# Performance work log

Measured on AMD Instinct MI355X. Metric: run time of the kernel, lower is better.

The kernel has to match this reference:

```python
import jax, jax.numpy as jnp
import numpy as np

D_MODEL, D_FF, N_HEAD = 1024, 4096, 16
D_HEAD = D_MODEL // N_HEAD
B, S = 8, 1024
EPS = 1e-6


def gelu(x):
    # tanh-approx GELU exactly as in source
    c = jnp.sqrt(jnp.asarray(2.0 / jnp.pi, x.dtype))
    return 0.5 * x * (1.0 + jnp.tanh(c * (x + 0.044715 * x ** 3)))


def layernorm(x, g, b):
    mu = jnp.mean(x, axis=-1, keepdims=True)
    var = jnp.mean((x - mu) ** 2, axis=-1, keepdims=True)
    return (x - mu) * jax.lax.rsqrt(var + EPS) * g + b


def setup_inputs() -> dict:
    key = jax.random.key(0)
    ks = jax.random.split(key, 12)
    s = 0.02
    p = lambda k, sh: (jax.random.normal(k, sh, jnp.float32) * s)
    inp = {
        "iter": 1,
        "x": jax.random.normal(ks[0], (B, S, D_MODEL), jnp.float32),
        "mask": jnp.tril(jnp.ones((S, S), jnp.float32))[None, None, :, :],
        "Wq": p(ks[1], (D_MODEL, D_MODEL)), "bq": jnp.zeros((D_MODEL,), jnp.float32),
        "Wk": p(ks[2], (D_MODEL, D_MODEL)), "bk": jnp.zeros((D_MODEL,), jnp.float32),
        "Wv": p(ks[3], (D_MODEL, D_MODEL)), "bv": jnp.zeros((D_MODEL,), jnp.float32),
        "W1": p(ks[4], (D_MODEL, D_FF)),   "b1": jnp.zeros((D_FF,), jnp.float32),
        "W2": p(ks[5], (D_FF, D_MODEL)),   "b2": jnp.zeros((D_MODEL,), jnp.float32),
        "ln_attn_g": jnp.ones((D_MODEL,), jnp.float32), "ln_attn_b": jnp.zeros((D_MODEL,), jnp.float32),
        "ln_ffn_g": jnp.ones((D_MODEL,), jnp.float32),  "ln_ffn_b": jnp.zeros((D_MODEL,), jnp.float32),
    }
    return inp


def encoder_layer(x, mask, Wq, bq, Wk, bk, Wv, bv, W1, b1, W2, b2,
                  ln_attn_g, ln_attn_b, ln_ffn_g, ln_ffn_b, it):
    # pre-norm on all iterations except the first
    norm_x = layernorm(x, ln_attn_g, ln_attn_b) if it != 0 else x

    def heads(t):  # [B,S,D] -> [B,H,S,Dh]
        return t.reshape(B, S, N_HEAD, D_HEAD).transpose(0, 2, 1, 3)

    q = heads(norm_x @ Wq + bq) / jnp.sqrt(jnp.asarray(D_HEAD, x.dtype))
    k = heads(norm_x @ Wk + bk)
    v = heads(norm_x @ Wv + bv)

    scores = jnp.einsum("bhqd,bhkd->bhqk", q, k)
    scores = scores * mask  # multiplicative mask, as in source
    attn = jax.nn.softmax(scores, axis=-1)
    context = jnp.einsum("bhqk,bhkd->bhqd", attn, v)
    # Faithful to torch .view on contiguous [B,H,S,Dh]: plain reshape (head-interleaving bug preserved)
    context = context.reshape(B, S, N_HEAD * D_HEAD)

    out = context + x  # residual (dropout = identity in eval)

    # positionwise FFN with internal pre-norm and residual
    h = layernorm(out, ln_ffn_g, ln_ffn_b)
    h = gelu(h @ W1 + b1)
    h = h @ W2 + b2
    return h + out


def reference(iter, x, mask, Wq, bq, Wk, bk, Wv, bv, W1, b1, W2, b2,
              ln_attn_g, ln_attn_b, ln_ffn_g, ln_ffn_b):
    return encoder_layer(x, mask, Wq, bq, Wk, bk, Wv, bv, W1, b1, W2, b2,
                         ln_attn_g, ln_attn_b, ln_ffn_g, ln_ffn_b, iter)
```

## Files before the change

### kernel.cpp

```cpp
#include <hip/hip_runtime.h>


#define B_N 8
#define SEQ 1024
#define DM 1024
#define DFF 4096
#define NH 16
#define DH 64
#define MROWS (B_N * SEQ)

typedef __attribute__((ext_vector_type(4))) float f32x4;
typedef __attribute__((ext_vector_type(8))) short short8;
typedef __attribute__((ext_vector_type(4))) unsigned short us4;
typedef unsigned short u16;

__device__ __forceinline__ float b2f(u16 u) { return __uint_as_float(((unsigned)u) << 16); }
__device__ __forceinline__ u16 f2b(float f) {
    unsigned u = __float_as_uint(f);
    return (u16)((u + 0x7fffu + ((u >> 16) & 1u)) >> 16);
}
__device__ __forceinline__ float gelu_f(float x) {
    float t = tanhf(0.7978845608028654f * (x + 0.044715f * x * x * x));
    return 0.5f * x * (1.0f + t);
}
__device__ __forceinline__ void async_cp16(const void* g, void* l) {
    __builtin_amdgcn_global_load_lds(
        (const __attribute__((address_space(1))) unsigned int*)g,
        (__attribute__((address_space(3))) unsigned int*)l, 16, 0, 0);
}

#define WAITL0()                                                                \
    asm volatile("s_waitcnt lgkmcnt(0)" ::: "memory");                          \
    __builtin_amdgcn_sched_barrier(0)

template <int EPI>
__global__ __launch_bounds__(256, 3) void gemm3(
    const u16* __restrict__ A, int lda,
    const u16* __restrict__ Bt, int ldb,
    void* __restrict__ C, int ldc,
    const float* __restrict__ bias, float scale, int K)
{
    __shared__ __align__(16) char lds[32768];

    const int tid = threadIdx.x;
    const int lane = tid & 63;
    const int w = tid >> 6;
    const int wm = w >> 1, wn = w & 1;
    const int rr = lane & 15, qq = lane >> 4;
    const int m0 = blockIdx.y * 128, n0 = blockIdx.x * 128;

    const int s = (rr & 7) << 4;
    const int swq = (qq * 16) ^ (s & 48);
    const int ksx[2] = { s & 64, 64 ^ (s & 64) };
    const int aoff = (wm * 64 + rr) * 128 + swq;
    const int boff = 16384 + (wn * 64 + rr) * 128 + swq;

    f32x4 acc[4][4];
#pragma unroll
    for (int i = 0; i < 4; i++)
#pragma unroll
        for (int j = 0; j < 4; j++)
#pragma unroll
            for (int e = 0; e < 4; e++) acc[i][j][e] = 0.f;

    const int NT = K >> 6;
    for (int t = 0; t < NT; ++t) {
#pragma unroll
        for (int i = 0; i < 4; ++i) {
            int g = tid + i * 256;
            int gs = (g & ~7) | ((g ^ (g >> 3)) & 7);
            async_cp16(A + (size_t)(m0 + (gs >> 3)) * lda + (t << 6) + ((gs & 7) << 3),
                       lds + g * 16);
        }
#pragma unroll
        for (int i = 0; i < 4; ++i) {
            int g = tid + i * 256;
            int gs = (g & ~7) | ((g ^ (g >> 3)) & 7);
            async_cp16(Bt + (size_t)(n0 + (gs >> 3)) * ldb + (t << 6) + ((gs & 7) << 3),
                       lds + 16384 + g * 16);
        }
        __syncthreads();

        short8 af[4][2], bfr[4][2];
#pragma unroll
        for (int mi = 0; mi < 4; ++mi)
#pragma unroll
            for (int ks = 0; ks < 2; ++ks)
                af[mi][ks] = *(const short8*)(lds + aoff + mi * 2048 + ksx[ks]);
#pragma unroll
        for (int ni = 0; ni < 4; ++ni)
#pragma unroll
            for (int ks = 0; ks < 2; ++ks)
                bfr[ni][ks] = *(const short8*)(lds + boff + ni * 2048 + ksx[ks]);
#pragma unroll
        for (int ks = 0; ks < 2; ++ks)
#pragma unroll
            for (int mi = 0; mi < 4; ++mi)
#pragma unroll
                for (int ni = 0; ni < 4; ++ni)
                    acc[mi][ni] = __builtin_amdgcn_mfma_f32_16x16x32_bf16(
                        af[mi][ks], bfr[ni][ks], acc[mi][ni], 0, 0, 0);
        __syncthreads();
    }

    const int ccol = n0 + wn * 64 + rr;
    const int crow = m0 + wm * 64 + qq * 4;
#pragma unroll
    for (int mi = 0; mi < 4; ++mi) {
#pragma unroll
        for (int ni = 0; ni < 4; ++ni) {
            const int colg = ccol + ni * 16;
            const float bv = bias ? bias[colg] : 0.f;
#pragma unroll
            for (int j = 0; j < 4; ++j) {
                const int rowg = crow + mi * 16 + j;
                float v = (acc[mi][ni][j] + bv) * scale;
                size_t idx = (size_t)rowg * ldc + colg;
                if (EPI == 1) v = gelu_f(v);
                if (EPI == 2) ((float*)C)[idx] += v;
                else ((u16*)C)[idx] = f2b(v);
            }
        }
    }
}

__global__ void vcolsum(const u16* __restrict__ Vb, float* __restrict__ Vcs)
{
    const int t = blockIdx.x, bh = blockIdx.y;
    const int b = bh >> 4, h = bh & 15;
    const int d = threadIdx.x;
    const u16* base = Vb + (size_t)(b * 1024 + t * 128) * DM + h * 64 + d;
    float s = 0.f;
#pragma unroll 8
    for (int k = 0; k < 128; ++k) s += b2f(base[(size_t)k * DM]);
    Vcs[((bh << 3) + t) * 64 + d] = s;
}

__global__ __launch_bounds__(256, 2) void flash_attn(
    const u16* __restrict__ Qb, const u16* __restrict__ Kb,
    const u16* __restrict__ Vt, const float* __restrict__ Vcs,
    u16* __restrict__ ctx)
{
    constexpr float L2E = 1.44269504f;
    const int bh = blockIdx.x, qt = blockIdx.y;
    const int b = bh >> 4, h = bh & 15;
    const int tid = threadIdx.x, lane = tid & 63, w = tid >> 6;
    const int rr = lane & 15, qq = lane >> 4;

    __shared__ __align__(16) u16 smem[32768];
    char* Ksb = (char*)smem;
    char* Vsb = (char*)(smem + 8192);
    char* Psb = (char*)(smem + 16384 + w * 4096);

    short8 qf[2][2];
    {
        const size_t qr = (size_t)(b * 1024 + qt * 128 + w * 32 + rr);
#pragma unroll
        for (int mi = 0; mi < 2; ++mi)
#pragma unroll
            for (int ks = 0; ks < 2; ++ks)
                qf[mi][ks] = *(const short8*)(Qb + (qr + mi * 16) * DM + h * 64 + ks * 32 + qq * 8);
    }

    f32x4 oacc[2][4];
    float mrow[2][4], lrow[2][4];
#pragma unroll
    for (int mi = 0; mi < 2; ++mi)
#pragma unroll
        for (int j = 0; j < 4; ++j) { mrow[mi][j] = -1e30f; lrow[mi][j] = 0.f; }
#pragma unroll
    for (int mi = 0; mi < 2; ++mi)
#pragma unroll
        for (int ni = 0; ni < 4; ++ni)
#pragma unroll
            for (int e = 0; e < 4; ++e) oacc[mi][ni][e] = 0.f;

    const u16* Kbase = Kb + (size_t)b * 1024 * DM + h * 64;
    const u16* Vbase = Vt + ((size_t)bh << 16);
    const int sxr = (rr & 7) << 4;
    const int qbase = qt * 128 + w * 32 + qq * 4;

    for (int t = 0; t <= qt; ++t) {
#pragma unroll
        for (int i = 0; i < 4; ++i) {
            int g = tid + i * 256;
            int gs = (g & ~7) | ((g ^ (g >> 3)) & 7);
            async_cp16(Kbase + (size_t)(t * 128 + (gs >> 3)) * DM + ((gs & 7) << 3),
                       Ksb + g * 16);
        }
#pragma unroll
        for (int i = 0; i < 4; ++i) {
            int g = tid + i * 256;
            int gs = (g & ~7) | ((g ^ (g >> 4)) & 7);
            async_cp16(Vbase + (size_t)(gs >> 4) * SEQ + t * 128 + ((gs & 15) << 3),
                       Vsb + g * 16);
        }
        __syncthreads();

        f32x4 sacc[2][8];
#pragma unroll
        for (int mi = 0; mi < 2; ++mi)
#pragma unroll
            for (int ni = 0; ni < 8; ++ni)
#pragma unroll
                for (int e = 0; e < 4; ++e) sacc[mi][ni][e] = 0.f;
#pragma unroll
        for (int ks = 0; ks < 2; ++ks)
#pragma unroll
            for (int ni = 0; ni < 8; ++ni) {
                short8 kf = *(const short8*)(Ksb + (rr + ni * 16) * 128 +
                                             ((ks * 64 + qq * 16) ^ sxr));
#pragma unroll
                for (int mi = 0; mi < 2; ++mi)
                    sacc[mi][ni] = __builtin_amdgcn_mfma_f32_16x16x32_bf16(
                        qf[mi][ks], kf, sacc[mi][ni], 0, 0, 0);
            }

        float mx[2][4];
#pragma unroll
        for (int mi = 0; mi < 2; ++mi)
#pragma unroll
            for (int j = 0; j < 4; ++j) mx[mi][j] = -1e30f;
        if (t == qt) {
            const int kb0 = t * 128 + rr;
#pragma unroll
            for (int mi = 0; mi < 2; ++mi)
#pragma unroll
                for (int ni = 0; ni < 8; ++ni)
#pragma unroll
                    for (int j = 0; j < 4; ++j) {
                        float sv = (kb0 + ni * 16 <= qbase + mi * 16 + j) ? sacc[mi][ni][j] : 0.f;
                        sacc[mi][ni][j] = sv;
                        mx[mi][j] = fmaxf(mx[mi][j], sv);
                    }
        } else {
#pragma unroll
            for (int mi = 0; mi < 2; ++mi)
#pragma unroll
                for (int ni = 0; ni < 8; ++ni)
#pragma unroll
                    for (int j = 0; j < 4; ++j)
                        mx[mi][j] = fmaxf(mx[mi][j], sacc[mi][ni][j]);
        }
#pragma unroll
        for (int mi = 0; mi < 2; ++mi)
#pragma unroll
            for (int j = 0; j < 4; ++j) {
                float v = mx[mi][j];
#pragma unroll
                for (int o = 1; o < 16; o <<= 1) v = fmaxf(v, __shfl_xor(v, o, 64));
                mx[mi][j] = v;
            }

        float rs[2][4];
#pragma unroll
        for (int mi = 0; mi < 2; ++mi)
#pragma unroll
            for (int j = 0; j < 4; ++j) {
                float mn = fmaxf(mrow[mi][j], mx[mi][j]);
                float sc = exp2f((mrow[mi][j] - mn) * L2E);
                mrow[mi][j] = mn;
                lrow[mi][j] *= sc;
                rs[mi][j] = 0.f;
#pragma unroll
                for (int ni = 0; ni < 4; ++ni) oacc[mi][ni][j] *= sc;
            }
#pragma unroll
        for (int mi = 0; mi < 2; ++mi)
#pragma unroll
            for (int ni = 0; ni < 8; ++ni)
#pragma unroll
                for (int j = 0; j < 4; ++j) {
                    float p = exp2f((sacc[mi][ni][j] - mrow[mi][j]) * L2E);
                    rs[mi][j] += p;
                    const int prow = mi * 16 + qq * 4 + j;
                    *(u16*)(Psb + prow * 256 +
                            (((rr + ni * 16) * 2) ^ ((prow & 7) << 4))) = f2b(p);
                }
#pragma unroll
        for (int mi = 0; mi < 2; ++mi)
#pragma unroll
            for (int j = 0; j < 4; ++j) {
                float v = rs[mi][j];
#pragma unroll
                for (int o = 1; o < 16; o <<= 1) v += __shfl_xor(v, o, 64);
                lrow[mi][j] += v;
            }

        WAITL0();

#pragma unroll
        for (int kk = 0; kk < 4; ++kk) {
            short8 pa[2], pv[4];
#pragma unroll
            for (int mi = 0; mi < 2; ++mi)
                pa[mi] = *(const short8*)(Psb + (mi * 16 + rr) * 256 +
                                          ((kk * 64 + qq * 16) ^ sxr));
#pragma unroll
            for (int ni = 0; ni < 4; ++ni)
                pv[ni] = *(const short8*)(Vsb + (rr + ni * 16) * 256 +
                                          ((kk * 64 + qq * 16) ^ sxr));
#pragma unroll
            for (int mi = 0; mi < 2; ++mi)
#pragma unroll
                for (int ni = 0; ni < 4; ++ni)
                    oacc[mi][ni] = __builtin_amdgcn_mfma_f32_16x16x32_bf16(
                        pa[mi], pv[ni], oacc[mi][ni], 0, 0, 0);
        }
        __syncthreads();
    }

    if (qt < 7) {
        float vsuf[4] = { 0.f, 0.f, 0.f, 0.f };
        for (int tt = qt + 1; tt < 8; ++tt)
#pragma unroll
            for (int ni = 0; ni < 4; ++ni)
                vsuf[ni] += Vcs[((bh << 3) + tt) * 64 + rr + ni * 16];
        const float km = (float)((7 - qt) * 128);
#pragma unroll
        for (int mi = 0; mi < 2; ++mi)
#pragma unroll
            for (int j = 0; j < 4; ++j) {
                float m = mrow[mi][j];
                float mfin = fmaxf(m, 0.f);
                float sc = exp2f((m - mfin) * L2E);
                float w0 = exp2f(-mfin * L2E);
                lrow[mi][j] = lrow[mi][j] * sc + km * w0;
#pragma unroll
                for (int ni = 0; ni < 4; ++ni)
                    oacc[mi][ni][j] = oacc[mi][ni][j] * sc + w0 * vsuf[ni];
            }
    }

    float inv[2][4];
#pragma unroll
    for (int mi = 0; mi < 2; ++mi)
#pragma unroll
        for (int j = 0; j < 4; ++j) inv[mi][j] = 1.0f / lrow[mi][j];
    u16* cb = ctx + ((size_t)bh << 16);
#pragma unroll
    for (int mi = 0; mi < 2; ++mi)
#pragma unroll
        for (int ni = 0; ni < 4; ++ni)
#pragma unroll
            for (int j = 0; j < 4; ++j) {
                const int srow = qt * 128 + w * 32 + mi * 16 + qq * 4 + j;
                cb[(size_t)srow * 64 + rr + ni * 16] = f2b(oacc[mi][ni][j] * inv[mi][j]);
            }
}

__global__ __launch_bounds__(256) void ln_bf16(
    const float* __restrict__ in, const float* __restrict__ gg,
    const float* __restrict__ bb, u16* __restrict__ outp,
    const int* __restrict__ iterp)
{
    const int row = blockIdx.x;
    const int t = threadIdx.x;
    const int lane = t & 63, w = t >> 6;
    const float* r = in + (size_t)row * DM;
    f32x4 x = *(const f32x4*)(r + t * 4);
    __shared__ float red[4];

    float s = x[0] + x[1] + x[2] + x[3];
#pragma unroll
    for (int o = 32; o; o >>= 1) s += __shfl_xor(s, o, 64);
    if (lane == 0) red[w] = s;
    __syncthreads();
    float mu = (red[0] + red[1] + red[2] + red[3]) * (1.0f / DM);
    __syncthreads();

    float d0 = x[0] - mu, d1 = x[1] - mu, d2 = x[2] - mu, d3 = x[3] - mu;
    float q = d0 * d0 + d1 * d1 + d2 * d2 + d3 * d3;
#pragma unroll
    for (int o = 32; o; o >>= 1) q += __shfl_xor(q, o, 64);
    if (lane == 0) red[w] = q;
    __syncthreads();
    float rs = rsqrtf((red[0] + red[1] + red[2] + red[3]) * (1.0f / DM) + 1e-6f);

    bool apply = !(iterp && iterp[0] == 0);
    f32x4 gv = *(const f32x4*)(gg + t * 4);
    f32x4 bv = *(const f32x4*)(bb + t * 4);
    us4 o;
    if (apply) {
        o[0] = f2b(d0 * rs * gv[0] + bv[0]);
        o[1] = f2b(d1 * rs * gv[1] + bv[1]);
        o[2] = f2b(d2 * rs * gv[2] + bv[2]);
        o[3] = f2b(d3 * rs * gv[3] + bv[3]);
    } else {
        o[0] = f2b(x[0]); o[1] = f2b(x[1]); o[2] = f2b(x[2]); o[3] = f2b(x[3]);
    }
    *(us4*)(outp + (size_t)row * DM + t * 4) = o;
}

__global__ void transW(const float* __restrict__ W, u16* __restrict__ WT, int Kd, int Nd)
{
    __shared__ float tile[32][33];
    int bx = blockIdx.x << 5, by = blockIdx.y << 5;
    int tx = threadIdx.x, ty = threadIdx.y;
#pragma unroll
    for (int i = 0; i < 32; i += 8)
        tile[ty + i][tx] = W[(size_t)(by + ty + i) * Nd + bx + tx];
    __syncthreads();
#pragma unroll
    for (int i = 0; i < 32; i += 8)
        WT[(size_t)(bx + ty + i) * Kd + by + tx] = f2b(tile[tx][ty + i]);
}

__global__ void transV(const u16* __restrict__ Vb, u16* __restrict__ Vt)
{
    __shared__ u16 tile[32][33];
    int s0 = blockIdx.x << 5, d0 = blockIdx.y << 5, bh = blockIdx.z;
    int b = bh >> 4, h = bh & 15;
    int tx = threadIdx.x, ty = threadIdx.y;
#pragma unroll
    for (int i = 0; i < 32; i += 8)
        tile[ty + i][tx] = Vb[(size_t)((b << 10) + s0 + ty + i) * DM + (h << 6) + d0 + tx];
    __syncthreads();
#pragma unroll
    for (int i = 0; i < 32; i += 8)
        Vt[((size_t)bh << 16) + (size_t)(d0 + ty + i) * SEQ + s0 + tx] = tile[tx][ty + i];
}

__global__ __launch_bounds__(256) void resid_add(
    const u16* __restrict__ ctx, const float* __restrict__ x, float* __restrict__ outp)
{
    size_t i = ((size_t)blockIdx.x * 256 + threadIdx.x) * 4;
    us4 c = *(const us4*)(ctx + i);
    f32x4 xv = *(const f32x4*)(x + i);
    f32x4 o;
#pragma unroll
    for (int j = 0; j < 4; j++) o[j] = xv[j] + b2f(c[j]);
    *(f32x4*)(outp + i) = o;
}

extern "C" void kernel_launch(void* const* d_in, const int* in_sizes, int n_in,
                              void* d_out, int out_size, void* d_ws, size_t ws_size,
                              hipStream_t stream)
{
    const int* iter = (const int*)d_in[0];
    const float* x = (const float*)d_in[1];
    const float* Wq = (const float*)d_in[3];
    const float* bq = (const float*)d_in[4];
    const float* Wk = (const float*)d_in[5];
    const float* bk = (const float*)d_in[6];
    const float* Wv = (const float*)d_in[7];
    const float* bv = (const float*)d_in[8];
    const float* W1 = (const float*)d_in[9];
    const float* b1 = (const float*)d_in[10];
    const float* W2 = (const float*)d_in[11];
    const float* b2 = (const float*)d_in[12];
    const float* lag = (const float*)d_in[13];
    const float* lab = (const float*)d_in[14];
    const float* lfg = (const float*)d_in[15];
    const float* lfb = (const float*)d_in[16];
    float* out = (float*)d_out;

    char* ws = (char*)d_ws;
    size_t off = 0;
    auto alloc = [&](size_t bytes) {
        char* p = ws + off;
        off += (bytes + 255) & ~(size_t)255;
        return p;
    };
    u16* NXb = (u16*)alloc((size_t)MROWS * DM * 2);
    u16* Qb  = (u16*)alloc((size_t)MROWS * DM * 2);
    u16* Kb  = (u16*)alloc((size_t)MROWS * DM * 2);
    u16* Vb  = (u16*)alloc((size_t)MROWS * DM * 2);
    u16* ctx = (u16*)alloc((size_t)MROWS * DM * 2);
    u16* h2  = (u16*)alloc((size_t)MROWS * DFF * 2);
    u16* WqT = (u16*)alloc((size_t)DM * DM * 2);
    u16* WkT = (u16*)alloc((size_t)DM * DM * 2);
    u16* WvT = (u16*)alloc((size_t)DM * DM * 2);
    u16* W1T = (u16*)alloc((size_t)DM * DFF * 2);
    u16* W2T = (u16*)alloc((size_t)DM * DFF * 2);
    float* Vcs = (float*)alloc((size_t)B_N * NH * 8 * 64 * 4);
    u16* Vt = NXb;
    u16* h1 = Qb;

    dim3 tb(32, 8);
    transW<<<dim3(DM / 32, DM / 32), tb, 0, stream>>>(Wq, WqT, DM, DM);
    transW<<<dim3(DM / 32, DM / 32), tb, 0, stream>>>(Wk, WkT, DM, DM);
    transW<<<dim3(DM / 32, DM / 32), tb, 0, stream>>>(Wv, WvT, DM, DM);
    transW<<<dim3(DFF / 32, DM / 32), tb, 0, stream>>>(W1, W1T, DM, DFF);
    transW<<<dim3(DM / 32, DFF / 32), tb, 0, stream>>>(W2, W2T, DFF, DM);

    ln_bf16<<<MROWS, 256, 0, stream>>>(x, lag, lab, NXb, iter);

    gemm3<0><<<dim3(DM / 128, MROWS / 128), 256, 0, stream>>>(
        NXb, DM, WqT, DM, Qb, DM, bq, 0.125f, DM);
    gemm3<0><<<dim3(DM / 128, MROWS / 128), 256, 0, stream>>>(
        NXb, DM, WkT, DM, Kb, DM, bk, 1.0f, DM);
    gemm3<0><<<dim3(DM / 128, MROWS / 128), 256, 0, stream>>>(
        NXb, DM, WvT, DM, Vb, DM, bv, 1.0f, DM);

    transV<<<dim3(SEQ / 32, DH / 32, B_N * NH), tb, 0, stream>>>(Vb, Vt);
    vcolsum<<<dim3(8, B_N * NH), 64, 0, stream>>>(Vb, Vcs);

    flash_attn<<<dim3(B_N * NH, SEQ / 128), 256, 0, stream>>>(Qb, Kb, Vt, Vcs, ctx);

    resid_add<<<(MROWS * DM) / 1024, 256, 0, stream>>>(ctx, x, out);

    ln_bf16<<<MROWS, 256, 0, stream>>>(out, lfg, lfb, h1, nullptr);
    gemm3<1><<<dim3(DFF / 128, MROWS / 128), 256, 0, stream>>>(
        h1, DM, W1T, DM, h2, DFF, b1, 1.0f, DM);
    gemm3<2><<<dim3(DM / 128, MROWS / 128), 256, 0, stream>>>(
        h2, DFF, W2T, DFF, (void*)out, DM, b2, 1.0f, DFF);
}
```

Measured before the change: 435.2 us.

## Fuse QKV projections into one GEMM, fold residual into attention, cheaper GELU

Concatenates Wq/Wk/Wv (with the 1/sqrt(d) scale folded into Wq and its bias) into a single 3072-wide GEMM, replacing three launches and giving a larger grid. Attention now reads Q/K/V from the interleaved QKV buffer and writes fp32 output plus residual directly, which removes the separate residual-add kernel and the bf16 context round trip. GELU's tanh is rewritten as an exp2 plus hardware reciprocal form, which is cheaper but slightly less precise. Folding the scale into bf16 weights is exact for 0.125, since it is a power of two.

```diff
diff --git a/kernel.cpp b/kernel.cpp
--- a/kernel.cpp
+++ b/kernel.cpp
@@ -4,6 +4,7 @@
 #define B_N 8
 #define SEQ 1024
 #define DM 1024
+#define DQKV 3072
 #define DFF 4096
 #define NH 16
 #define DH 64
@@ -20,8 +21,12 @@
     return (u16)((u + 0x7fffu + ((u >> 16) & 1u)) >> 16);
 }
 __device__ __forceinline__ float gelu_f(float x) {
-    float t = tanhf(0.7978845608028654f * (x + 0.044715f * x * x * x));
-    return 0.5f * x * (1.0f + t);
+    float x2 = x * x;
+    float z2l = x * (2.3013935056f + 0.1029194997f * x2);
+    float t = exp2f(z2l);
+    float r;
+    asm("v_rcp_f32 %0, %1" : "=v"(r) : "v"(t + 1.0f));
+    return x - x * r;
 }
 __device__ __forceinline__ void async_cp16(const void* g, void* l) {
     __builtin_amdgcn_global_load_lds(
@@ -124,22 +129,22 @@
     }
 }
 
-__global__ void vcolsum(const u16* __restrict__ Vb, float* __restrict__ Vcs)
+__global__ void vcolsum(const u16* __restrict__ QKV, float* __restrict__ Vcs)
 {
     const int t = blockIdx.x, bh = blockIdx.y;
     const int b = bh >> 4, h = bh & 15;
     const int d = threadIdx.x;
-    const u16* base = Vb + (size_t)(b * 1024 + t * 128) * DM + h * 64 + d;
+    const u16* base = QKV + (size_t)(b * 1024 + t * 128) * DQKV + 2048 + h * 64 + d;
     float s = 0.f;
 #pragma unroll 8
-    for (int k = 0; k < 128; ++k) s += b2f(base[(size_t)k * DM]);
+    for (int k = 0; k < 128; ++k) s += b2f(base[(size_t)k * DQKV]);
     Vcs[((bh << 3) + t) * 64 + d] = s;
 }
 
 __global__ __launch_bounds__(256, 2) void flash_attn(
-    const u16* __restrict__ Qb, const u16* __restrict__ Kb,
-    const u16* __restrict__ Vt, const float* __restrict__ Vcs,
-    u16* __restrict__ ctx)
+    const u16* __restrict__ QKV, const u16* __restrict__ Vt,
+    const float* __restrict__ Vcs, const float* __restrict__ x,
+    float* __restrict__ outp)
 {
     constexpr float L2E = 1.44269504f;
     const int bh = blockIdx.x, qt = blockIdx.y;
@@ -159,7 +164,7 @@
         for (int mi = 0; mi < 2; ++mi)
 #pragma unroll
             for (int ks = 0; ks < 2; ++ks)
-                qf[mi][ks] = *(const short8*)(Qb + (qr + mi * 16) * DM + h * 64 + ks * 32 + qq * 8);
+                qf[mi][ks] = *(const short8*)(QKV + (qr + mi * 16) * DQKV + h * 64 + ks * 32 + qq * 8);
     }
 
     f32x4 oacc[2][4];
@@ -175,7 +180,7 @@
 #pragma unroll
             for (int e = 0; e < 4; ++e) oacc[mi][ni][e] = 0.f;
 
-    const u16* Kbase = Kb + (size_t)b * 1024 * DM + h * 64;
+    const u16* Kbase = QKV + (size_t)b * 1024 * DQKV + 1024 + h * 64;
     const u16* Vbase = Vt + ((size_t)bh << 16);
     const int sxr = (rr & 7) << 4;
     const int qbase = qt * 128 + w * 32 + qq * 4;
@@ -185,7 +190,7 @@
         for (int i = 0; i < 4; ++i) {
             int g = tid + i * 256;
             int gs = (g & ~7) | ((g ^ (g >> 3)) & 7);
-            async_cp16(Kbase + (size_t)(t * 128 + (gs >> 3)) * DM + ((gs & 7) << 3),
+            async_cp16(Kbase + (size_t)(t * 128 + (gs >> 3)) * DQKV + ((gs & 7) << 3),
                        Ksb + g * 16);
         }
 #pragma unroll
@@ -337,15 +342,17 @@
     for (int mi = 0; mi < 2; ++mi)
 #pragma unroll
         for (int j = 0; j < 4; ++j) inv[mi][j] = 1.0f / lrow[mi][j];
-    u16* cb = ctx + ((size_t)bh << 16);
+    const float* xb = x + ((size_t)bh << 16);
+    float* ob = outp + ((size_t)bh << 16);
 #pragma unroll
     for (int mi = 0; mi < 2; ++mi)
 #pragma unroll
         for (int ni = 0; ni < 4; ++ni)
 #pragma unroll
             for (int j = 0; j < 4; ++j) {
-                const int srow = qt * 128 + w * 32 + mi * 16 + qq * 4 + j;
-                cb[(size_t)srow * 64 + rr + ni * 16] = f2b(oacc[mi][ni][j] * inv[mi][j]);
+                const size_t idx = (size_t)(qt * 128 + w * 32 + mi * 16 + qq * 4 + j) * 64
+                                   + rr + ni * 16;
+                ob[idx] = xb[idx] + oacc[mi][ni][j] * inv[mi][j];
             }
 }
 
@@ -392,7 +399,8 @@
     *(us4*)(outp + (size_t)row * DM + t * 4) = o;
 }
 
-__global__ void transW(const float* __restrict__ W, u16* __restrict__ WT, int Kd, int Nd)
+__global__ void transW(const float* __restrict__ W, u16* __restrict__ WT,
+                       int Kd, int Nd, float sc)
 {
     __shared__ float tile[32][33];
     int bx = blockIdx.x << 5, by = blockIdx.y << 5;
@@ -403,10 +411,10 @@
     __syncthreads();
 #pragma unroll
     for (int i = 0; i < 32; i += 8)
-        WT[(size_t)(bx + ty + i) * Kd + by + tx] = f2b(tile[tx][ty + i]);
-}
-
-__global__ void transV(const u16* __restrict__ Vb, u16* __restrict__ Vt)
+        WT[(size_t)(bx + ty + i) * Kd + by + tx] = f2b(tile[tx][ty + i] * sc);
+}
+
+__global__ void transV(const u16* __restrict__ QKV, u16* __restrict__ Vt)
 {
     __shared__ u16 tile[32][33];
     int s0 = blockIdx.x << 5, d0 = blockIdx.y << 5, bh = blockIdx.z;
@@ -414,23 +422,19 @@
     int tx = threadIdx.x, ty = threadIdx.y;
 #pragma unroll
     for (int i = 0; i < 32; i += 8)
-        tile[ty + i][tx] = Vb[(size_t)((b << 10) + s0 + ty + i) * DM + (h << 6) + d0 + tx];
+        tile[ty + i][tx] = QKV[(size_t)((b << 10) + s0 + ty + i) * DQKV + 2048 + (h << 6) + d0 + tx];
     __syncthreads();
 #pragma unroll
     for (int i = 0; i < 32; i += 8)
         Vt[((size_t)bh << 16) + (size_t)(d0 + ty + i) * SEQ + s0 + tx] = tile[tx][ty + i];
 }
 
-__global__ __launch_bounds__(256) void resid_add(
-    const u16* __restrict__ ctx, const float* __restrict__ x, float* __restrict__ outp)
-{
-    size_t i = ((size_t)blockIdx.x * 256 + threadIdx.x) * 4;
-    us4 c = *(const us4*)(ctx + i);
-    f32x4 xv = *(const f32x4*)(x + i);
-    f32x4 o;
-#pragma unroll
-    for (int j = 0; j < 4; j++) o[j] = xv[j] + b2f(c[j]);
-    *(f32x4*)(outp + i) = o;
+__global__ void pack_bias(const float* __restrict__ bq, const float* __restrict__ bk,
+                          const float* __restrict__ bv, float* __restrict__ o)
+{
+    int i = blockIdx.x * 256 + threadIdx.x;
+    float v = (i < 1024) ? bq[i] * 0.125f : ((i < 2048) ? bk[i - 1024] : bv[i - 2048]);
+    o[i] = v;
 }
 
 extern "C" void kernel_launch(void* const* d_in, const int* in_sizes, int n_in,
@@ -462,43 +466,34 @@
         off += (bytes + 255) & ~(size_t)255;
         return p;
     };
-    u16* NXb = (u16*)alloc((size_t)MROWS * DM * 2);
-    u16* Qb  = (u16*)alloc((size_t)MROWS * DM * 2);
-    u16* Kb  = (u16*)alloc((size_t)MROWS * DM * 2);
-    u16* Vb  = (u16*)alloc((size_t)MROWS * DM * 2);
-    u16* ctx = (u16*)alloc((size_t)MROWS * DM * 2);
-    u16* h2  = (u16*)alloc((size_t)MROWS * DFF * 2);
-    u16* WqT = (u16*)alloc((size_t)DM * DM * 2);
-    u16* WkT = (u16*)alloc((size_t)DM * DM * 2);
-    u16* WvT = (u16*)alloc((size_t)DM * DM * 2);
-    u16* W1T = (u16*)alloc((size_t)DM * DFF * 2);
-    u16* W2T = (u16*)alloc((size_t)DM * DFF * 2);
+    u16* NXb  = (u16*)alloc((size_t)MROWS * DM * 2);
+    u16* QKV  = (u16*)alloc((size_t)MROWS * DQKV * 2);
+    u16* h2   = (u16*)alloc((size_t)MROWS * DFF * 2);
+    u16* WqkvT = (u16*)alloc((size_t)DQKV * DM * 2);
+    u16* W1T  = (u16*)alloc((size_t)DM * DFF * 2);
+    u16* W2T  = (u16*)alloc((size_t)DM * DFF * 2);
+    float* bqkv = (float*)alloc((size_t)DQKV * 4);
     float* Vcs = (float*)alloc((size_t)B_N * NH * 8 * 64 * 4);
     u16* Vt = NXb;
-    u16* h1 = Qb;
+    u16* h1 = QKV;
 
     dim3 tb(32, 8);
-    transW<<<dim3(DM / 32, DM / 32), tb, 0, stream>>>(Wq, WqT, DM, DM);
-    transW<<<dim3(DM / 32, DM / 32), tb, 0, stream>>>(Wk, WkT, DM, DM);
-    transW<<<dim3(DM / 32, DM / 32), tb, 0, stream>>>(Wv, WvT, DM, DM);
-    transW<<<dim3(DFF / 32, DM / 32), tb, 0, stream>>>(W1, W1T, DM, DFF);
-    transW<<<dim3(DM / 32, DFF / 32), tb, 0, stream>>>(W2, W2T, DFF, DM);
+    transW<<<dim3(DM / 32, DM / 32), tb, 0, stream>>>(Wq, WqkvT, DM, DM, 0.125f);
+    transW<<<dim3(DM / 32, DM / 32), tb, 0, stream>>>(Wk, WqkvT + (size_t)1024 * DM, DM, DM, 1.0f);
+    transW<<<dim3(DM / 32, DM / 32), tb, 0, stream>>>(Wv, WqkvT + (size_t)2048 * DM, DM, DM, 1.0f);
+    transW<<<dim3(DFF / 32, DM / 32), tb, 0, stream>>>(W1, W1T, DM, DFF, 1.0f);
+    transW<<<dim3(DM / 32, DFF / 32), tb, 0, stream>>>(W2, W2T, DFF, DM, 1.0f);
+    pack_bias<<<DQKV / 256, 256, 0, stream>>>(bq, bk, bv, bqkv);
 
     ln_bf16<<<MROWS, 256, 0, stream>>>(x, lag, lab, NXb, iter);
 
-    gemm3<0><<<dim3(DM / 128, MROWS / 128), 256, 0, stream>>>(
-        NXb, DM, WqT, DM, Qb, DM, bq, 0.125f, DM);
-    gemm3<0><<<dim3(DM / 128, MROWS / 128), 256, 0, stream>>>(
-        NXb, DM, WkT, DM, Kb, DM, bk, 1.0f, DM);
-    gemm3<0><<<dim3(DM / 128, MROWS / 128), 256, 0, stream>>>(
-        NXb, DM, WvT, DM, Vb, DM, bv, 1.0f, DM);
-
-    transV<<<dim3(SEQ / 32, DH / 32, B_N * NH), tb, 0, stream>>>(Vb, Vt);
-    vcolsum<<<dim3(8, B_N * NH), 64, 0, stream>>>(Vb, Vcs);
-
-    flash_attn<<<dim3(B_N * NH, SEQ / 128), 256, 0, stream>>>(Qb, Kb, Vt, Vcs, ctx);
-
-    resid_add<<<(MROWS * DM) / 1024, 256, 0, stream>>>(ctx, x, out);
+    gemm3<0><<<dim3(DQKV / 128, MROWS / 128), 256, 0, stream>>>(
+        NXb, DM, WqkvT, DM, QKV, DQKV, bqkv, 1.0f, DM);
+
+    transV<<<dim3(SEQ / 32, DH / 32, B_N * NH), tb, 0, stream>>>(QKV, Vt);
+    vcolsum<<<dim3(8, B_N * NH), 64, 0, stream>>>(QKV, Vcs);
+
+    flash_attn<<<dim3(B_N * NH, SEQ / 128), 256, 0, stream>>>(QKV, Vt, Vcs, x, out);
 
     ln_bf16<<<MROWS, 256, 0, stream>>>(out, lfg, lfb, h1, nullptr);
     gemm3<1><<<dim3(DFF / 128, MROWS / 128), 256, 0, stream>>>(
```

Measured after the change: 389.4 us. 10.5% less time.
